# Kernel tuning notes

Hardware: AMD Instinct MI355X
Metric: run time of the kernel (lower is better)

Reference implementation:

```python
import jax, jax.numpy as jnp
import numpy as np

N, D, NUM_CLASSES = 8192, 128, 128
ALPHA = 1.0
K = 16


def setup_inputs() -> dict:
    key = jax.random.key(0)
    k1, k2 = jax.random.split(key)
    inputs = jax.random.normal(k1, (N, D), dtype=jnp.float32)
    targets = jax.random.randint(k2, (N,), 0, NUM_CLASSES, dtype=jnp.int64)
    return {"inputs": inputs, "targets": targets}


def knn_softmax(inputs, targets, alpha=ALPHA, k=K):
    n = inputs.shape[0]
    # pairwise euclidean distances (GEMM-based), clamped like the original
    sq = jnp.sum(inputs * inputs, axis=1)                      # [n]
    d2 = sq[:, None] + sq[None, :] - 2.0 * (inputs @ inputs.T)  # [n,n]
    dist = jnp.sqrt(jnp.maximum(d2, 1e-12))

    eye = jnp.eye(n, dtype=bool)
    same = targets[:, None] == targets[None, :]
    pos_mask = same & ~eye          # same label, off-diagonal
    neg_mask = ~same                # different label (diagonal excluded automatically)

    # per-row threshold: (K+1)-th smallest off-diagonal distance
    dm = jnp.where(eye, jnp.inf, dist)
    neg_topk, _ = jax.lax.top_k(-dm, k + 1)   # k+1 smallest (negated)
    thr = -neg_topk[:, k]                      # [n]

    below = dist < thr[:, None]
    pos_sel = pos_mask & below
    neg_sel = neg_mask & below

    exp_d = jnp.exp(-alpha * dist)
    pos_logit = jnp.sum(jnp.where(pos_sel, exp_d, 0.0), axis=1)  # [n]
    neg_logit = jnp.sum(jnp.where(neg_sel, exp_d, 0.0), axis=1)  # [n]
    count_pos = jnp.sum(pos_sel, axis=1)
    count_neg = jnp.sum(neg_sel, axis=1)

    # fallback when no positive falls below the threshold: use the first positive pair
    first_pos = jnp.argmax(pos_mask, axis=1)                     # [n]
    fb_dist = jnp.take_along_axis(dist, first_pos[:, None], axis=1)[:, 0]
    fallback = jnp.exp(-alpha * fb_dist)
    pos_eff = jnp.where(count_pos == 0, fallback, pos_logit)

    # rows with no positives or no negatives at all are skipped (`continue`)
    valid = pos_mask.any(axis=1) & neg_mask.any(axis=1)

    loss_i = -jnp.log(pos_eff / (pos_eff + neg_logit))
    loss = jnp.sum(jnp.where(valid, loss_i, 0.0)) / n

    count_pos_acc = jnp.where(count_pos == 0, 1, count_pos)  # fallback gives len 1
    accuracy = jnp.sum((valid & (count_pos_acc > count_neg)).astype(jnp.float32)) / n
    tp = jnp.sum(jnp.where(valid, count_pos, 0)).astype(jnp.float32) / n
    tn = jnp.sum(jnp.where(valid, count_neg, 0)).astype(jnp.float32) / n
    return loss, accuracy, tp, tn


def reference(inputs, targets):
    return knn_softmax(inputs, targets)
```

## Files before the change

### kernel.cpp

```cpp
#include <hip/hip_runtime.h>

#define NPTS 8192
#define DIM 128
#define NCLS 128
#define KSEL 17
#define RB   64
#define NIT  32
#define CAPW 40
#define SEG  32
#define NSEG 8
#define MBLK 1024
#define BIG 3.0e38f

typedef short bf16x8 __attribute__((ext_vector_type(8)));
typedef float f32x4 __attribute__((ext_vector_type(4)));

__device__ __forceinline__ unsigned short f2bf(float f) {
  unsigned int u = __float_as_uint(f);
  u += 0x7fffu + ((u >> 16) & 1u);
  return (unsigned short)(u >> 16);
}

__device__ __forceinline__ unsigned flipF(float f) {
  unsigned u = __float_as_uint(f);
  return (u & 0x80000000u) ? ~u : (u | 0x80000000u);
}
__device__ __forceinline__ float unflipF(unsigned k) {
  unsigned u = (k & 0x80000000u) ? (k & 0x7fffffffu) : ~k;
  return __uint_as_float(u);
}

__device__ __forceinline__ float kth17_4(float a, float b, float c, float d) {
  const unsigned ka = flipF(a), kb = flipF(b), kc = flipF(c), kd = flipF(d);
  unsigned ans = 0x80000000u;
  for (int bit = 30; bit >= 0; --bit) {
    unsigned mid = ans | (1u << bit);
    int cc = __popcll(__ballot(ka < mid)) + __popcll(__ballot(kb < mid)) +
             __popcll(__ballot(kc < mid)) + __popcll(__ballot(kd < mid));
    if (cc < KSEL) ans = mid;
  }
  return unflipF(ans);
}

__global__ void prep(const float* __restrict__ X, const long long* __restrict__ targets,
                     unsigned short* __restrict__ Xb, float* __restrict__ sqv,
                     int* __restrict__ tgt, int* __restrict__ ccount,
                     int* __restrict__ j0a, int* __restrict__ j1a) {
  const int tid = threadIdx.x;
  if (blockIdx.x == 2048) {
    __shared__ int cc[NCLS], c0[NCLS], c1[NCLS];
    if (tid < NCLS) { cc[tid] = 0; c0[tid] = 0x7fffffff; c1[tid] = 0x7fffffff; }
    __syncthreads();
    for (int base = tid * 4; base < NPTS; base += 1024) {
      const long long* p = targets + base;
#pragma unroll
      for (int k = 0; k < 4; k++) {
        int c = (int)p[k];
        tgt[base + k] = c;
        atomicAdd(&cc[c], 1);
        atomicMin(&c0[c], base + k);
      }
    }
    __syncthreads();
    for (int base = tid * 4; base < NPTS; base += 1024) {
#pragma unroll
      for (int k = 0; k < 4; k++) {
        int c = tgt[base + k];
        if (base + k != c0[c]) atomicMin(&c1[c], base + k);
      }
    }
    __syncthreads();
    if (tid < NCLS) { ccount[tid] = cc[tid]; j0a[tid] = c0[tid]; j1a[tid] = c1[tid]; }
    return;
  }
  const int w = tid >> 6, lane = tid & 63;
  const int gw = blockIdx.x * 4 + w;
  const float* xr = X + (size_t)gw * DIM;
  float a = xr[lane], b = xr[lane + 64];
  Xb[(size_t)gw * DIM + lane] = f2bf(a);
  Xb[(size_t)gw * DIM + lane + 64] = f2bf(b);
  float s = a * a + b * b;
#pragma unroll
  for (int off = 32; off; off >>= 1) s += __shfl_xor(s, off);
  if (lane == 0) sqv[gw] = s;
}

__global__ __launch_bounds__(256, 4) void knn_main(
    const unsigned short* __restrict__ Xb, const float* __restrict__ sqv,
    const int* __restrict__ tgt, float* __restrict__ scr, int* __restrict__ cscr) {
  __shared__ __align__(16) unsigned short shB[2][4096];
  __shared__ __align__(16) float shPub[RB * CAPW];
  __shared__ int cntL[RB];

  const int tid = threadIdx.x;
  const int w = tid >> 6;
  const int lane = tid & 63;
  const int quad = lane >> 4;
  const int l16 = lane & 15;
  const int rg = blockIdx.x >> 3;
  const int eighth = blockIdx.x & 7;
  const int rbase = rg * RB;
  const int cbase = eighth * 1024;

  const int w0off = (tid << 5) ^ (((tid >> 3) & 7) << 4);
  const unsigned lmlt = (1u << l16) - 1;
  int rdoff[4];
#pragma unroll
  for (int kb = 0; kb < 4; kb++)
    rdoff[kb] = (l16 * 256 + quad * 16 + kb * 64) ^ ((l16 & 7) << 4);

  bf16x8 afrag[4];
  {
    const unsigned short* arow = Xb + (size_t)(rbase + w * 16 + l16) * DIM + quad * 8;
#pragma unroll
    for (int kb = 0; kb < 4; kb++) afrag[kb] = *(const bf16x8*)(arow + kb * 32);
  }
  float sqi[4]; int ti[4];
#pragma unroll
  for (int r = 0; r < 4; r++) {
    int rr = rbase + w * 16 + quad * 4 + r;
    sqi[r] = sqv[rr]; ti[r] = tgt[rr];
  }
  int tdw;
  {
    int d = rbase + w * 16 - cbase;
    tdw = (d >= 0 && d < 1024) ? (d >> 4) : -1;
  }

  const unsigned short* gtile0 = Xb + (size_t)cbase * DIM;
  const float* sqp = sqv + cbase + l16;
  const int*   tgp = tgt + cbase + l16;

  float m1[4], m2[4];
#pragma unroll
  for (int r = 0; r < 4; r++) { m1[r] = BIG; m2[r] = BIG; }
  {
    bf16x8 s0 = *(const bf16x8*)(gtile0 + tid * 16);
    bf16x8 s1 = *(const bf16x8*)(gtile0 + tid * 16 + 8);
    *(bf16x8*)((char*)&shB[0][0] + w0off) = s0;
    *(bf16x8*)((char*)&shB[0][0] + (w0off ^ 16)) = s1;
  }
  float sq0 = sqp[0], sq1 = sqp[16];
  __syncthreads();
  for (int j = 0; j < NIT; j++) {
    const int jn = (j + 1) & (NIT - 1);
    const unsigned short* src = gtile0 + (size_t)jn * 4096;
    bf16x8 s0 = *(const bf16x8*)(src + tid * 16);
    bf16x8 s1 = *(const bf16x8*)(src + tid * 16 + 8);
    const float nsq0 = sqp[jn * 32], nsq1 = sqp[jn * 32 + 16];
    const char* lb = (const char*)&shB[j & 1][0];
    bf16x8 b0[4], b1[4];
#pragma unroll
    for (int kb = 0; kb < 4; kb++) {
      b0[kb] = *(const bf16x8*)(lb + rdoff[kb]);
      b1[kb] = *(const bf16x8*)(lb + rdoff[kb] + 4096);
    }
    f32x4 a0 = {0.f, 0.f, 0.f, 0.f}, a1 = {0.f, 0.f, 0.f, 0.f};
#pragma unroll
    for (int kb = 0; kb < 4; kb++) {
      a0 = __builtin_amdgcn_mfma_f32_16x16x32_bf16(afrag[kb], b0[kb], a0, 0, 0, 0);
      a1 = __builtin_amdgcn_mfma_f32_16x16x32_bf16(afrag[kb], b1[kb], a1, 0, 0, 0);
    }
    float v0[4], v1[4];
#pragma unroll
    for (int r = 0; r < 4; r++) {
      v0[r] = fmaf(-2.0f, a0[r], sq0);
      v1[r] = fmaf(-2.0f, a1[r], sq1);
    }
    if ((unsigned)(tdw - 2 * j) < 2u) {
#pragma unroll
      for (int r = 0; r < 4; r++) {
        if (2 * j == tdw && l16 == quad * 4 + r) v0[r] = BIG;
        if (2 * j + 1 == tdw && l16 == quad * 4 + r) v1[r] = BIG;
      }
    }
#pragma unroll
    for (int r = 0; r < 4; r++) {
      m2[r] = fminf(m2[r], fmaxf(m1[r], v0[r]));
      m1[r] = fminf(m1[r], v0[r]);
      m2[r] = fminf(m2[r], fmaxf(m1[r], v1[r]));
      m1[r] = fminf(m1[r], v1[r]);
    }
    sq0 = nsq0; sq1 = nsq1;
    char* wb = (char*)&shB[(j & 1) ^ 1][0];
    *(bf16x8*)(wb + w0off) = s0;
    *(bf16x8*)(wb + (w0off ^ 16)) = s1;
    __syncthreads();
  }

#pragma unroll
  for (int r = 0; r < 4; r++) {
    const int row = w * 16 + quad * 4 + r;
    shPub[row * 32 + l16 * 2] = m1[r];
    shPub[row * 32 + l16 * 2 + 1] = m2[r];
  }
  __syncthreads();
  float Ur[4] = {0.f, 0.f, 0.f, 0.f};
  for (int rp = 0; rp < 16; rp += 2) {
    const int li = lane & 31;
    const unsigned ka = (lane < 32) ? flipF(shPub[(w * 16 + rp) * 32 + li]) : 0xFFFFFFFFu;
    const unsigned kb2 = (lane < 32) ? flipF(shPub[(w * 16 + rp + 1) * 32 + li]) : 0xFFFFFFFFu;
    unsigned ansA = 0u, ansB = 0u;
    for (int bit = 31; bit >= 14; --bit) {
      const unsigned mA = ansA | (1u << bit), mB = ansB | (1u << bit);
      const int ca = __popcll(__ballot(ka < mA));
      const int cb = __popcll(__ballot(kb2 < mB));
      if (ca < KSEL) ansA = mA;
      if (cb < KSEL) ansB = mB;
    }
    const float ua = unflipF(ansA | 0x3FFFu), ub = unflipF(ansB | 0x3FFFu);
#pragma unroll
    for (int r = 0; r < 4; r++) {
      const int myrow = quad * 4 + r;
      if (myrow == rp) Ur[r] = ua;
      if (myrow == rp + 1) Ur[r] = ub;
    }
  }

  float* bufD = shPub;
  int cntr[4] = {0, 0, 0, 0};
  {
    bf16x8 s0 = *(const bf16x8*)(gtile0 + tid * 16);
    bf16x8 s1 = *(const bf16x8*)(gtile0 + tid * 16 + 8);
    *(bf16x8*)((char*)&shB[0][0] + w0off) = s0;
    *(bf16x8*)((char*)&shB[0][0] + (w0off ^ 16)) = s1;
  }
  sq0 = sqp[0]; sq1 = sqp[16];
  int tj0 = tgp[0], tj1 = tgp[16];
  __syncthreads();
  for (int j = 0; j < NIT; j++) {
    const int jn = (j + 1) & (NIT - 1);
    const unsigned short* src = gtile0 + (size_t)jn * 4096;
    bf16x8 s0 = *(const bf16x8*)(src + tid * 16);
    bf16x8 s1 = *(const bf16x8*)(src + tid * 16 + 8);
    const float nsq0 = sqp[jn * 32], nsq1 = sqp[jn * 32 + 16];
    const int ntj0 = tgp[jn * 32], ntj1 = tgp[jn * 32 + 16];
    const char* lb = (const char*)&shB[j & 1][0];
    bf16x8 b0[4], b1[4];
#pragma unroll
    for (int kb = 0; kb < 4; kb++) {
      b0[kb] = *(const bf16x8*)(lb + rdoff[kb]);
      b1[kb] = *(const bf16x8*)(lb + rdoff[kb] + 4096);
    }
    f32x4 a0 = {0.f, 0.f, 0.f, 0.f}, a1 = {0.f, 0.f, 0.f, 0.f};
#pragma unroll
    for (int kb = 0; kb < 4; kb++) {
      a0 = __builtin_amdgcn_mfma_f32_16x16x32_bf16(afrag[kb], b0[kb], a0, 0, 0, 0);
      a1 = __builtin_amdgcn_mfma_f32_16x16x32_bf16(afrag[kb], b1[kb], a1, 0, 0, 0);
    }
    float v0[4], v1[4];
#pragma unroll
    for (int r = 0; r < 4; r++) {
      v0[r] = fmaf(-2.0f, a0[r], sq0);
      v1[r] = fmaf(-2.0f, a1[r], sq1);
    }
    if ((unsigned)(tdw - 2 * j) < 2u) {
#pragma unroll
      for (int r = 0; r < 4; r++) {
        if (2 * j == tdw && l16 == quad * 4 + r) v0[r] = BIG;
        if (2 * j + 1 == tdw && l16 == quad * 4 + r) v1[r] = BIG;
      }
    }
#pragma unroll
    for (int r = 0; r < 4; r++) {
      {
        const bool p = (v0[r] <= Ur[r]);
        const unsigned long long bal = __ballot(p);
        if (bal) {
          const unsigned qm = (unsigned)(bal >> (quad << 4)) & 0xFFFFu;
          const int pos = cntr[r] + __popc(qm & lmlt);
          if (p && pos < CAPW) {
            unsigned enc = __float_as_uint(fmaxf(v0[r] + sqi[r], 0.0f));
            if (tj0 == ti[r]) enc |= 0x80000000u;
            bufD[(w * 16 + quad * 4 + r) * CAPW + pos] = __uint_as_float(enc);
          }
          cntr[r] += __popc(qm);
        }
      }
      {
        const bool p = (v1[r] <= Ur[r]);
        const unsigned long long bal = __ballot(p);
        if (bal) {
          const unsigned qm = (unsigned)(bal >> (quad << 4)) & 0xFFFFu;
          const int pos = cntr[r] + __popc(qm & lmlt);
          if (p && pos < CAPW) {
            unsigned enc = __float_as_uint(fmaxf(v1[r] + sqi[r], 0.0f));
            if (tj1 == ti[r]) enc |= 0x80000000u;
            bufD[(w * 16 + quad * 4 + r) * CAPW + pos] = __uint_as_float(enc);
          }
          cntr[r] += __popc(qm);
        }
      }
    }
    sq0 = nsq0; sq1 = nsq1; tj0 = ntj0; tj1 = ntj1;
    char* wb = (char*)&shB[(j & 1) ^ 1][0];
    *(bf16x8*)(wb + w0off) = s0;
    *(bf16x8*)(wb + (w0off ^ 16)) = s1;
    __syncthreads();
  }
#pragma unroll
  for (int r = 0; r < 4; r++)
    if (l16 == 0) cntL[w * 16 + quad * 4 + r] = cntr[r];
  __syncthreads();

  for (int rl = 0; rl < 16; rl++) {
    const int grow = rbase + w * 16 + rl;
    const int tot = cntL[w * 16 + rl];
    float* srow = scr + (size_t)grow * (NSEG * SEG) + eighth * SEG;
    if (tot <= SEG) {
      if (lane < tot) srow[lane] = bufD[(w * 16 + rl) * CAPW + lane];
      if (lane == 0) cscr[grow * NSEG + eighth] = tot;
    } else {
      const int n = min(tot, CAPW);
      float e = BIG; int m = 0;
      if (lane < n) {
        unsigned u = __float_as_uint(bufD[(w * 16 + rl) * CAPW + lane]);
        m = (int)(u >> 31); e = __uint_as_float(u & 0x7fffffffu);
      }
      for (int round = 0; round < KSEL; round++) {
        float vv = e; int idx = lane;
#pragma unroll
        for (int off = 32; off; off >>= 1) {
          float ov = __shfl_xor(vv, off);
          int   oi = __shfl_xor(idx, off);
          if (ov < vv || (ov == vv && oi < idx)) { vv = ov; idx = oi; }
        }
        if (idx == lane) {
          unsigned ub = __float_as_uint(e);
          if (m) ub |= 0x80000000u;
          srow[round] = __uint_as_float(ub);
          e = BIG;
        }
      }
      if (lane == 0) cscr[grow * NSEG + eighth] = KSEL;
    }
  }
}

__global__ __launch_bounds__(256) void knn_merge(
    const float* __restrict__ scr, const int* __restrict__ cscr,
    const float* __restrict__ sqv, const int* __restrict__ tgt,
    const int* __restrict__ ccount, const int* __restrict__ j0a,
    const int* __restrict__ j1a, const float* __restrict__ X32,
    float* __restrict__ pacc) {
  __shared__ float blockAcc[4];
  const int tid = threadIdx.x;
  const int w = tid >> 6;
  const int lane = tid & 63;
  if (tid < 4) blockAcc[tid] = 0.0f;
  __syncthreads();
  for (int ri = 0; ri < 2; ri++) {
    const int grow = blockIdx.x * 8 + w * 2 + ri;
    const float* srow = scr + (size_t)grow * (NSEG * SEG);
    const int h = lane >> 5, li = lane & 31;
    float e[4]; int mm[4];
#pragma unroll
    for (int j = 0; j < 4; j++) {
      const int seg = j * 2 + h;
      const int cj = cscr[grow * NSEG + seg];
      if (li < cj) {
        unsigned u = __float_as_uint(srow[seg * SEG + li]);
        mm[j] = (int)(u >> 31); e[j] = __uint_as_float(u & 0x7fffffffu);
      } else { e[j] = BIG; mm[j] = 0; }
    }
    const float t17 = kth17_4(e[0], e[1], e[2], e[3]);
    float pls = 0.0f, nls = 0.0f; int cp = 0, cn = 0;
#pragma unroll
    for (int j = 0; j < 4; j++) {
      const bool s = (e[j] < t17);
      const float x = s ? expf(-sqrtf(fmaxf(e[j], 1e-12f))) : 0.0f;
      if (mm[j]) { pls += x; cp += (int)s; }
      else       { nls += x; cn += (int)s; }
    }
    int cpn = cp * 65536 + cn;
#pragma unroll
    for (int off = 32; off; off >>= 1) {
      pls += __shfl_xor(pls, off); nls += __shfl_xor(nls, off);
      cpn += __shfl_xor(cpn, off);
    }
    const int cpt = cpn >> 16, cnt_ = cpn & 0xffff;
    const int c = tgt[grow];
    const int ncl = ccount[c];
    const bool valid = (ncl > 1) && (ncl < NPTS);
    if (valid) {
      float pos_eff;
      if (cpt == 0) {
        const int jf = (grow == j0a[c]) ? j1a[c] : j0a[c];
        const float* xi = X32 + (size_t)grow * DIM;
        const float* xj = X32 + (size_t)jf * DIM;
        float pp = xi[lane] * xj[lane] + xi[lane + 64] * xj[lane + 64];
#pragma unroll
        for (int off = 32; off; off >>= 1) pp += __shfl_xor(pp, off);
        const float fb2 = sqv[grow] + sqv[jf] - 2.0f * pp;
        pos_eff = expf(-sqrtf(fmaxf(fb2, 1e-12f)));
      } else {
        pos_eff = pls;
      }
      if (lane == 0) {
        const float loss_i = -logf(pos_eff / (pos_eff + nls));
        const int cpa = (cpt == 0) ? 1 : cpt;
        atomicAdd(&blockAcc[0], loss_i);
        atomicAdd(&blockAcc[1], (cpa > cnt_) ? 1.0f : 0.0f);
        atomicAdd(&blockAcc[2], (float)cpt);
        atomicAdd(&blockAcc[3], (float)cnt_);
      }
    }
  }
  __syncthreads();
  if (tid < 4) pacc[blockIdx.x * 4 + tid] = blockAcc[tid];
}

__global__ void fin(const float* __restrict__ pacc, float* __restrict__ out) {
  __shared__ float red[256];
  const int tid = threadIdx.x;
  const int c = tid & 3, b0 = tid >> 2;
  float s = 0.0f;
  for (int b = b0; b < MBLK; b += 64) s += pacc[b * 4 + c];
  red[tid] = s;
  __syncthreads();
  if (tid < 4) {
    float t = 0.0f;
    for (int i = tid; i < 256; i += 4) t += red[i];
    out[tid] = t * (1.0f / (float)NPTS);
  }
}

extern "C" void kernel_launch(void* const* d_in, const int* in_sizes, int n_in,
                              void* d_out, int out_size, void* d_ws, size_t ws_size,
                              hipStream_t stream) {
  const float* X = (const float*)d_in[0];
  const long long* targets = (const long long*)d_in[1];
  float* out = (float*)d_out;

  char* ws = (char*)d_ws;
  unsigned short* Xb = (unsigned short*)ws;
  float* sqv    = (float*)   (ws + (2u << 20));
  int*   tgt    = (int*)     (ws + (2u << 20) + (32u << 10));
  int*   ccount = (int*)     (ws + (2u << 20) + (64u << 10));
  int*   j0a    = (int*)     (ws + (2u << 20) + (65u << 10));
  int*   j1a    = (int*)     (ws + (2u << 20) + (66u << 10));
  float* pacc   = (float*)   (ws + (2u << 20) + (68u << 10));
  float* scr = (float*)(ws + (2u << 20) + (128u << 10));
  int* cscr  = (int*)  (ws + (2u << 20) + (128u << 10) +
                        (size_t)NPTS * NSEG * SEG * 4);

  prep<<<2049, 256, 0, stream>>>(X, targets, Xb, sqv, tgt, ccount, j0a, j1a);
  knn_main<<<1024, 256, 0, stream>>>(Xb, sqv, tgt, scr, cscr);
  knn_merge<<<MBLK, 256, 0, stream>>>(scr, cscr, sqv, tgt, ccount, j0a, j1a, X, pacc);
  fin<<<1, 256, 0, stream>>>(pacc, out);
}
```

Measured before the change: 174.1 us.

## Double row tile per block and stage column tiles via direct global-to-LDS loads

Each block now covers 128 rows instead of 64, so each wave holds two A fragments and reuses every B fragment read from LDS for two MFMAs, halving LDS traffic per MFMA. Column tiles are copied with global_load_lds straight into LDS, with the swizzle moved to the source address, instead of going through registers. The buffer filled in the last iteration of the first pass is reused as the first tile of the second pass. Second-minimum tracking now uses fmed3. In exchange the grid is halved to 512 blocks with launch bounds of 2 blocks per SM, which lowers occupancy and latency hiding and raises register pressure.

```diff
diff --git a/kernel.cpp b/kernel.cpp
--- a/kernel.cpp
+++ b/kernel.cpp
@@ -4,7 +4,7 @@
 #define DIM 128
 #define NCLS 128
 #define KSEL 17
-#define RB   64
+#define RB   128
 #define NIT  32
 #define CAPW 40
 #define SEG  32
@@ -85,7 +85,7 @@
   if (lane == 0) sqv[gw] = s;
 }
 
-__global__ __launch_bounds__(256, 4) void knn_main(
+__global__ __launch_bounds__(256, 2) void knn_main(
     const unsigned short* __restrict__ Xb, const float* __restrict__ sqv,
     const int* __restrict__ tgt, float* __restrict__ scr, int* __restrict__ cscr) {
   __shared__ __align__(16) unsigned short shB[2][4096];
@@ -102,104 +102,132 @@
   const int rbase = rg * RB;
   const int cbase = eighth * 1024;
 
-  const int w0off = (tid << 5) ^ (((tid >> 3) & 7) << 4);
   const unsigned lmlt = (1u << l16) - 1;
   int rdoff[4];
 #pragma unroll
   for (int kb = 0; kb < 4; kb++)
     rdoff[kb] = (l16 * 256 + quad * 16 + kb * 64) ^ ((l16 & 7) << 4);
 
-  bf16x8 afrag[4];
-  {
-    const unsigned short* arow = Xb + (size_t)(rbase + w * 16 + l16) * DIM + quad * 8;
-#pragma unroll
-    for (int kb = 0; kb < 4; kb++) afrag[kb] = *(const bf16x8*)(arow + kb * 32);
-  }
-  float sqi[4]; int ti[4];
-#pragma unroll
-  for (int r = 0; r < 4; r++) {
-    int rr = rbase + w * 16 + quad * 4 + r;
-    sqi[r] = sqv[rr]; ti[r] = tgt[rr];
-  }
-  int tdw;
-  {
-    int d = rbase + w * 16 - cbase;
-    tdw = (d >= 0 && d < 1024) ? (d >> 4) : -1;
-  }
-
-  const unsigned short* gtile0 = Xb + (size_t)cbase * DIM;
+  const int g0 = w * 128 + lane;
+  const int g1 = w * 128 + 64 + lane;
+  const int soff0 = (g0 ^ ((g0 >> 4) & 7)) * 16;
+  const int soff1 = (g1 ^ ((g1 >> 4) & 7)) * 16;
+  const int ldst0 = (w * 128) * 16;
+  const int ldst1 = (w * 128 + 64) * 16;
+
+  const char* gslab0 = (const char*)(Xb) + (size_t)cbase * DIM * 2;
+  auto stage = [&](int buf, int j) {
+    const char* src = gslab0 + (size_t)j * 8192;
+    __builtin_amdgcn_global_load_lds((const unsigned int*)(src + soff0),
+                                     (unsigned int*)((char*)&shB[buf][0] + ldst0),
+                                     16, 0, 0);
+    __builtin_amdgcn_global_load_lds((const unsigned int*)(src + soff1),
+                                     (unsigned int*)((char*)&shB[buf][0] + ldst1),
+                                     16, 0, 0);
+  };
+
+  bf16x8 afrag[2][4];
+#pragma unroll
+  for (int s = 0; s < 2; s++) {
+    const unsigned short* arow =
+        Xb + (size_t)(rbase + w * 32 + s * 16 + l16) * DIM + quad * 8;
+#pragma unroll
+    for (int kb = 0; kb < 4; kb++) afrag[s][kb] = *(const bf16x8*)(arow + kb * 32);
+  }
+  float sqi[2][4]; int ti[2][4];
+#pragma unroll
+  for (int s = 0; s < 2; s++)
+#pragma unroll
+    for (int r = 0; r < 4; r++) {
+      int rr = rbase + w * 32 + s * 16 + quad * 4 + r;
+      sqi[s][r] = sqv[rr]; ti[s][r] = tgt[rr];
+    }
+  int tdw[2];
+#pragma unroll
+  for (int s = 0; s < 2; s++) {
+    int d = rbase + w * 32 + s * 16 - cbase;
+    tdw[s] = (d >= 0 && d < 1024) ? (d >> 4) : -1;
+  }
+
   const float* sqp = sqv + cbase + l16;
   const int*   tgp = tgt + cbase + l16;
 
-  float m1[4], m2[4];
-#pragma unroll
-  for (int r = 0; r < 4; r++) { m1[r] = BIG; m2[r] = BIG; }
-  {
-    bf16x8 s0 = *(const bf16x8*)(gtile0 + tid * 16);
-    bf16x8 s1 = *(const bf16x8*)(gtile0 + tid * 16 + 8);
-    *(bf16x8*)((char*)&shB[0][0] + w0off) = s0;
-    *(bf16x8*)((char*)&shB[0][0] + (w0off ^ 16)) = s1;
-  }
-  float sq0 = sqp[0], sq1 = sqp[16];
+  float m1[2][4], m2[2][4];
+#pragma unroll
+  for (int s = 0; s < 2; s++)
+#pragma unroll
+    for (int r = 0; r < 4; r++) { m1[s][r] = BIG; m2[s][r] = BIG; }
+  stage(0, 0);
   __syncthreads();
   for (int j = 0; j < NIT; j++) {
-    const int jn = (j + 1) & (NIT - 1);
-    const unsigned short* src = gtile0 + (size_t)jn * 4096;
-    bf16x8 s0 = *(const bf16x8*)(src + tid * 16);
-    bf16x8 s1 = *(const bf16x8*)(src + tid * 16 + 8);
-    const float nsq0 = sqp[jn * 32], nsq1 = sqp[jn * 32 + 16];
+    const int jn = (j + 1 < NIT) ? j + 1 : 0;
+    stage((j & 1) ^ 1, jn);
+    const float sq0 = sqp[j * 32], sq1 = sqp[j * 32 + 16];
     const char* lb = (const char*)&shB[j & 1][0];
-    bf16x8 b0[4], b1[4];
-#pragma unroll
-    for (int kb = 0; kb < 4; kb++) {
-      b0[kb] = *(const bf16x8*)(lb + rdoff[kb]);
-      b1[kb] = *(const bf16x8*)(lb + rdoff[kb] + 4096);
-    }
-    f32x4 a0 = {0.f, 0.f, 0.f, 0.f}, a1 = {0.f, 0.f, 0.f, 0.f};
-#pragma unroll
-    for (int kb = 0; kb < 4; kb++) {
-      a0 = __builtin_amdgcn_mfma_f32_16x16x32_bf16(afrag[kb], b0[kb], a0, 0, 0, 0);
-      a1 = __builtin_amdgcn_mfma_f32_16x16x32_bf16(afrag[kb], b1[kb], a1, 0, 0, 0);
-    }
-    float v0[4], v1[4];
+    f32x4 a00 = {0.f,0.f,0.f,0.f}, a10 = {0.f,0.f,0.f,0.f};
+    f32x4 a01 = {0.f,0.f,0.f,0.f}, a11 = {0.f,0.f,0.f,0.f};
+    {
+      bf16x8 b[4];
+#pragma unroll
+      for (int kb = 0; kb < 4; kb++) b[kb] = *(const bf16x8*)(lb + rdoff[kb]);
+#pragma unroll
+      for (int kb = 0; kb < 4; kb++) {
+        a00 = __builtin_amdgcn_mfma_f32_16x16x32_bf16(afrag[0][kb], b[kb], a00, 0, 0, 0);
+        a10 = __builtin_amdgcn_mfma_f32_16x16x32_bf16(afrag[1][kb], b[kb], a10, 0, 0, 0);
+      }
+    }
+    {
+      bf16x8 b[4];
+#pragma unroll
+      for (int kb = 0; kb < 4; kb++) b[kb] = *(const bf16x8*)(lb + rdoff[kb] + 4096);
+#pragma unroll
+      for (int kb = 0; kb < 4; kb++) {
+        a01 = __builtin_amdgcn_mfma_f32_16x16x32_bf16(afrag[0][kb], b[kb], a01, 0, 0, 0);
+        a11 = __builtin_amdgcn_mfma_f32_16x16x32_bf16(afrag[1][kb], b[kb], a11, 0, 0, 0);
+      }
+    }
+    float v0[2][4], v1[2][4];
+#pragma unroll
+    for (int s = 0; s < 2; s++)
+#pragma unroll
+      for (int r = 0; r < 4; r++) {
+        v0[s][r] = fmaf(-2.0f, s ? a10[r] : a00[r], sq0);
+        v1[s][r] = fmaf(-2.0f, s ? a11[r] : a01[r], sq1);
+      }
+    if (((unsigned)(tdw[0] - 2 * j) < 2u) || ((unsigned)(tdw[1] - 2 * j) < 2u)) {
+#pragma unroll
+      for (int s = 0; s < 2; s++)
+#pragma unroll
+        for (int r = 0; r < 4; r++) {
+          if (2 * j == tdw[s] && l16 == quad * 4 + r) v0[s][r] = BIG;
+          if (2 * j + 1 == tdw[s] && l16 == quad * 4 + r) v1[s][r] = BIG;
+        }
+    }
+#pragma unroll
+    for (int s = 0; s < 2; s++)
+#pragma unroll
+      for (int r = 0; r < 4; r++) {
+        m2[s][r] = __builtin_amdgcn_fmed3f(m1[s][r], m2[s][r], v0[s][r]);
+        m1[s][r] = fminf(m1[s][r], v0[s][r]);
+        m2[s][r] = __builtin_amdgcn_fmed3f(m1[s][r], m2[s][r], v1[s][r]);
+        m1[s][r] = fminf(m1[s][r], v1[s][r]);
+      }
+    __syncthreads();
+  }
+
+#pragma unroll
+  for (int s = 0; s < 2; s++)
 #pragma unroll
     for (int r = 0; r < 4; r++) {
-      v0[r] = fmaf(-2.0f, a0[r], sq0);
-      v1[r] = fmaf(-2.0f, a1[r], sq1);
-    }
-    if ((unsigned)(tdw - 2 * j) < 2u) {
-#pragma unroll
-      for (int r = 0; r < 4; r++) {
-        if (2 * j == tdw && l16 == quad * 4 + r) v0[r] = BIG;
-        if (2 * j + 1 == tdw && l16 == quad * 4 + r) v1[r] = BIG;
-      }
-    }
-#pragma unroll
-    for (int r = 0; r < 4; r++) {
-      m2[r] = fminf(m2[r], fmaxf(m1[r], v0[r]));
-      m1[r] = fminf(m1[r], v0[r]);
-      m2[r] = fminf(m2[r], fmaxf(m1[r], v1[r]));
-      m1[r] = fminf(m1[r], v1[r]);
-    }
-    sq0 = nsq0; sq1 = nsq1;
-    char* wb = (char*)&shB[(j & 1) ^ 1][0];
-    *(bf16x8*)(wb + w0off) = s0;
-    *(bf16x8*)(wb + (w0off ^ 16)) = s1;
-    __syncthreads();
-  }
-
-#pragma unroll
-  for (int r = 0; r < 4; r++) {
-    const int row = w * 16 + quad * 4 + r;
-    shPub[row * 32 + l16 * 2] = m1[r];
-    shPub[row * 32 + l16 * 2 + 1] = m2[r];
-  }
-  __syncthreads();
-  float Ur[4] = {0.f, 0.f, 0.f, 0.f};
-  for (int rp = 0; rp < 16; rp += 2) {
+      const int row = w * 32 + s * 16 + quad * 4 + r;
+      shPub[row * 32 + l16 * 2] = m1[s][r];
+      shPub[row * 32 + l16 * 2 + 1] = m2[s][r];
+    }
+  float Ur[2][4];
+  for (int rp = 0; rp < 32; rp += 2) {
     const int li = lane & 31;
-    const unsigned ka = (lane < 32) ? flipF(shPub[(w * 16 + rp) * 32 + li]) : 0xFFFFFFFFu;
-    const unsigned kb2 = (lane < 32) ? flipF(shPub[(w * 16 + rp + 1) * 32 + li]) : 0xFFFFFFFFu;
+    const unsigned ka  = (lane < 32) ? flipF(shPub[(w * 32 + rp) * 32 + li]) : 0xFFFFFFFFu;
+    const unsigned kb2 = (lane < 32) ? flipF(shPub[(w * 32 + rp + 1) * 32 + li]) : 0xFFFFFFFFu;
     unsigned ansA = 0u, ansB = 0u;
     for (int bit = 31; bit >= 14; --bit) {
       const unsigned mA = ansA | (1u << bit), mB = ansB | (1u << bit);
@@ -210,111 +238,121 @@
     }
     const float ua = unflipF(ansA | 0x3FFFu), ub = unflipF(ansB | 0x3FFFu);
 #pragma unroll
-    for (int r = 0; r < 4; r++) {
-      const int myrow = quad * 4 + r;
-      if (myrow == rp) Ur[r] = ua;
-      if (myrow == rp + 1) Ur[r] = ub;
-    }
+    for (int s = 0; s < 2; s++)
+#pragma unroll
+      for (int r = 0; r < 4; r++) {
+        const int myrow = s * 16 + quad * 4 + r;
+        if (myrow == rp) Ur[s][r] = ua;
+        if (myrow == rp + 1) Ur[s][r] = ub;
+      }
   }
 
   float* bufD = shPub;
-  int cntr[4] = {0, 0, 0, 0};
-  {
-    bf16x8 s0 = *(const bf16x8*)(gtile0 + tid * 16);
-    bf16x8 s1 = *(const bf16x8*)(gtile0 + tid * 16 + 8);
-    *(bf16x8*)((char*)&shB[0][0] + w0off) = s0;
-    *(bf16x8*)((char*)&shB[0][0] + (w0off ^ 16)) = s1;
-  }
-  sq0 = sqp[0]; sq1 = sqp[16];
-  int tj0 = tgp[0], tj1 = tgp[16];
+  int cntr[2][4];
+#pragma unroll
+  for (int s = 0; s < 2; s++)
+#pragma unroll
+    for (int r = 0; r < 4; r++) cntr[s][r] = 0;
+  for (int j = 0; j < NIT; j++) {
+    const int jn = (j + 1 < NIT) ? j + 1 : 0;
+    stage((j & 1) ^ 1, jn);
+    const float sq0 = sqp[j * 32], sq1 = sqp[j * 32 + 16];
+    const int tj0 = tgp[j * 32], tj1 = tgp[j * 32 + 16];
+    const char* lb = (const char*)&shB[j & 1][0];
+    f32x4 a00 = {0.f,0.f,0.f,0.f}, a10 = {0.f,0.f,0.f,0.f};
+    f32x4 a01 = {0.f,0.f,0.f,0.f}, a11 = {0.f,0.f,0.f,0.f};
+    {
+      bf16x8 b[4];
+#pragma unroll
+      for (int kb = 0; kb < 4; kb++) b[kb] = *(const bf16x8*)(lb + rdoff[kb]);
+#pragma unroll
+      for (int kb = 0; kb < 4; kb++) {
+        a00 = __builtin_amdgcn_mfma_f32_16x16x32_bf16(afrag[0][kb], b[kb], a00, 0, 0, 0);
+        a10 = __builtin_amdgcn_mfma_f32_16x16x32_bf16(afrag[1][kb], b[kb], a10, 0, 0, 0);
+      }
+    }
+    {
+      bf16x8 b[4];
+#pragma unroll
+      for (int kb = 0; kb < 4; kb++) b[kb] = *(const bf16x8*)(lb + rdoff[kb] + 4096);
+#pragma unroll
+      for (int kb = 0; kb < 4; kb++) {
+        a01 = __builtin_amdgcn_mfma_f32_16x16x32_bf16(afrag[0][kb], b[kb], a01, 0, 0, 0);
+        a11 = __builtin_amdgcn_mfma_f32_16x16x32_bf16(afrag[1][kb], b[kb], a11, 0, 0, 0);
+      }
+    }
+    float v0[2][4], v1[2][4];
+#pragma unroll
+    for (int s = 0; s < 2; s++)
+#pragma unroll
+      for (int r = 0; r < 4; r++) {
+        v0[s][r] = fmaf(-2.0f, s ? a10[r] : a00[r], sq0);
+        v1[s][r] = fmaf(-2.0f, s ? a11[r] : a01[r], sq1);
+      }
+    if (((unsigned)(tdw[0] - 2 * j) < 2u) || ((unsigned)(tdw[1] - 2 * j) < 2u)) {
+#pragma unroll
+      for (int s = 0; s < 2; s++)
+#pragma unroll
+        for (int r = 0; r < 4; r++) {
+          if (2 * j == tdw[s] && l16 == quad * 4 + r) v0[s][r] = BIG;
+          if (2 * j + 1 == tdw[s] && l16 == quad * 4 + r) v1[s][r] = BIG;
+        }
+    }
+#pragma unroll
+    for (int s = 0; s < 2; s++)
+#pragma unroll
+      for (int r = 0; r < 4; r++) {
+        {
+          const bool p = (v0[s][r] <= Ur[s][r]);
+          const unsigned long long bal = __ballot(p);
+          if (bal) {
+            const unsigned qm = (unsigned)(bal >> (quad << 4)) & 0xFFFFu;
+            const int pos = cntr[s][r] + __popc(qm & lmlt);
+            if (p && pos < CAPW) {
+              unsigned enc = __float_as_uint(fmaxf(v0[s][r] + sqi[s][r], 0.0f));
+              if (tj0 == ti[s][r]) enc |= 0x80000000u;
+              bufD[(w * 32 + s * 16 + quad * 4 + r) * CAPW + pos] = __uint_as_float(enc);
+            }
+            cntr[s][r] += __popc(qm);
+          }
+        }
+        {
+          const bool p = (v1[s][r] <= Ur[s][r]);
+          const unsigned long long bal = __ballot(p);
+          if (bal) {
+            const unsigned qm = (unsigned)(bal >> (quad << 4)) & 0xFFFFu;
+            const int pos = cntr[s][r] + __popc(qm & lmlt);
+            if (p && pos < CAPW) {
+              unsigned enc = __float_as_uint(fmaxf(v1[s][r] + sqi[s][r], 0.0f));
+              if (tj1 == ti[s][r]) enc |= 0x80000000u;
+              bufD[(w * 32 + s * 16 + quad * 4 + r) * CAPW + pos] = __uint_as_float(enc);
+            }
+            cntr[s][r] += __popc(qm);
+          }
+        }
+      }
+    __syncthreads();
+  }
+#pragma unroll
+  for (int s = 0; s < 2; s++)
+#pragma unroll
+    for (int r = 0; r < 4; r++)
+      if (l16 == 0) cntL[w * 32 + s * 16 + quad * 4 + r] = cntr[s][r];
   __syncthreads();
-  for (int j = 0; j < NIT; j++) {
-    const int jn = (j + 1) & (NIT - 1);
-    const unsigned short* src = gtile0 + (size_t)jn * 4096;
-    bf16x8 s0 = *(const bf16x8*)(src + tid * 16);
-    bf16x8 s1 = *(const bf16x8*)(src + tid * 16 + 8);
-    const float nsq0 = sqp[jn * 32], nsq1 = sqp[jn * 32 + 16];
-    const int ntj0 = tgp[jn * 32], ntj1 = tgp[jn * 32 + 16];
-    const char* lb = (const char*)&shB[j & 1][0];
-    bf16x8 b0[4], b1[4];
-#pragma unroll
-    for (int kb = 0; kb < 4; kb++) {
-      b0[kb] = *(const bf16x8*)(lb + rdoff[kb]);
-      b1[kb] = *(const bf16x8*)(lb + rdoff[kb] + 4096);
-    }
-    f32x4 a0 = {0.f, 0.f, 0.f, 0.f}, a1 = {0.f, 0.f, 0.f, 0.f};
-#pragma unroll
-    for (int kb = 0; kb < 4; kb++) {
-      a0 = __builtin_amdgcn_mfma_f32_16x16x32_bf16(afrag[kb], b0[kb], a0, 0, 0, 0);
-      a1 = __builtin_amdgcn_mfma_f32_16x16x32_bf16(afrag[kb], b1[kb], a1, 0, 0, 0);
-    }
-    float v0[4], v1[4];
-#pragma unroll
-    for (int r = 0; r < 4; r++) {
-      v0[r] = fmaf(-2.0f, a0[r], sq0);
-      v1[r] = fmaf(-2.0f, a1[r], sq1);
-    }
-    if ((unsigned)(tdw - 2 * j) < 2u) {
-#pragma unroll
-      for (int r = 0; r < 4; r++) {
-        if (2 * j == tdw && l16 == quad * 4 + r) v0[r] = BIG;
-        if (2 * j + 1 == tdw && l16 == quad * 4 + r) v1[r] = BIG;
-      }
-    }
-#pragma unroll
-    for (int r = 0; r < 4; r++) {
-      {
-        const bool p = (v0[r] <= Ur[r]);
-        const unsigned long long bal = __ballot(p);
-        if (bal) {
-          const unsigned qm = (unsigned)(bal >> (quad << 4)) & 0xFFFFu;
-          const int pos = cntr[r] + __popc(qm & lmlt);
-          if (p && pos < CAPW) {
-            unsigned enc = __float_as_uint(fmaxf(v0[r] + sqi[r], 0.0f));
-            if (tj0 == ti[r]) enc |= 0x80000000u;
-            bufD[(w * 16 + quad * 4 + r) * CAPW + pos] = __uint_as_float(enc);
-          }
-          cntr[r] += __popc(qm);
-        }
-      }
-      {
-        const bool p = (v1[r] <= Ur[r]);
-        const unsigned long long bal = __ballot(p);
-        if (bal) {
-          const unsigned qm = (unsigned)(bal >> (quad << 4)) & 0xFFFFu;
-          const int pos = cntr[r] + __popc(qm & lmlt);
-          if (p && pos < CAPW) {
-            unsigned enc = __float_as_uint(fmaxf(v1[r] + sqi[r], 0.0f));
-            if (tj1 == ti[r]) enc |= 0x80000000u;
-            bufD[(w * 16 + quad * 4 + r) * CAPW + pos] = __uint_as_float(enc);
-          }
-          cntr[r] += __popc(qm);
-        }
-      }
-    }
-    sq0 = nsq0; sq1 = nsq1; tj0 = ntj0; tj1 = ntj1;
-    char* wb = (char*)&shB[(j & 1) ^ 1][0];
-    *(bf16x8*)(wb + w0off) = s0;
-    *(bf16x8*)(wb + (w0off ^ 16)) = s1;
-    __syncthreads();
-  }
-#pragma unroll
-  for (int r = 0; r < 4; r++)
-    if (l16 == 0) cntL[w * 16 + quad * 4 + r] = cntr[r];
-  __syncthreads();
-
-  for (int rl = 0; rl < 16; rl++) {
-    const int grow = rbase + w * 16 + rl;
-    const int tot = cntL[w * 16 + rl];
+
+  for (int rl = 0; rl < 32; rl++) {
+    const int row = w * 32 + rl;
+    const int grow = rbase + row;
+    const int tot = cntL[row];
     float* srow = scr + (size_t)grow * (NSEG * SEG) + eighth * SEG;
     if (tot <= SEG) {
-      if (lane < tot) srow[lane] = bufD[(w * 16 + rl) * CAPW + lane];
+      if (lane < tot) srow[lane] = bufD[row * CAPW + lane];
       if (lane == 0) cscr[grow * NSEG + eighth] = tot;
     } else {
       const int n = min(tot, CAPW);
       float e = BIG; int m = 0;
       if (lane < n) {
-        unsigned u = __float_as_uint(bufD[(w * 16 + rl) * CAPW + lane]);
+        unsigned u = __float_as_uint(bufD[row * CAPW + lane]);
         m = (int)(u >> 31); e = __uint_as_float(u & 0x7fffffffu);
       }
       for (int round = 0; round < KSEL; round++) {
@@ -445,7 +483,7 @@
                         (size_t)NPTS * NSEG * SEG * 4);
 
   prep<<<2049, 256, 0, stream>>>(X, targets, Xb, sqv, tgt, ccount, j0a, j1a);
-  knn_main<<<1024, 256, 0, stream>>>(Xb, sqv, tgt, scr, cscr);
+  knn_main<<<512, 256, 0, stream>>>(Xb, sqv, tgt, scr, cscr);
   knn_merge<<<MBLK, 256, 0, stream>>>(scr, cscr, sqv, tgt, ccount, j0a, j1a, X, pacc);
   fin<<<1, 256, 0, stream>>>(pacc, out);
 }
```

Result: slower. 189.9 us (+9.1%).

## Stage B tiles via direct global-to-LDS loads and use med3 for top-2 update

Applied to the files above, without the earlier changes.

Replaces the register-staged global→LDS copy of the column tiles with __builtin_amdgcn_global_load_lds direct loads, issued one tile ahead into the double buffer. The XOR swizzle moves from the LDS write address to the global source address. The sq and target values are now loaded for the current tile rather than prefetched. It also replaces the min/max pair in the running top-2 update with fmed3, splits the B fragment reads into two halves to lower register pressure, and drops one barrier between the min pass and the threshold search. This is meant to cut VGPR use and per-iteration copy instructions, but it relies on the async LDS loads being visible after the barrier and on the barrier removal being safe.

```diff
diff --git a/kernel.cpp b/kernel.cpp
--- a/kernel.cpp
+++ b/kernel.cpp
@@ -102,12 +102,29 @@
   const int rbase = rg * RB;
   const int cbase = eighth * 1024;
 
-  const int w0off = (tid << 5) ^ (((tid >> 3) & 7) << 4);
   const unsigned lmlt = (1u << l16) - 1;
   int rdoff[4];
 #pragma unroll
   for (int kb = 0; kb < 4; kb++)
     rdoff[kb] = (l16 * 256 + quad * 16 + kb * 64) ^ ((l16 & 7) << 4);
+
+  const int g0 = w * 128 + lane;
+  const int g1 = w * 128 + 64 + lane;
+  const int soff0 = (g0 ^ ((g0 >> 4) & 7)) * 16;
+  const int soff1 = (g1 ^ ((g1 >> 4) & 7)) * 16;
+  const int ldst0 = (w * 128) * 16;
+  const int ldst1 = (w * 128 + 64) * 16;
+
+  const char* gslab0 = (const char*)(Xb) + (size_t)cbase * DIM * 2;
+  auto stage = [&](int buf, int j) {
+    const char* src = gslab0 + (size_t)j * 8192;
+    __builtin_amdgcn_global_load_lds((const unsigned int*)(src + soff0),
+                                     (unsigned int*)((char*)&shB[buf][0] + ldst0),
+                                     16, 0, 0);
+    __builtin_amdgcn_global_load_lds((const unsigned int*)(src + soff1),
+                                     (unsigned int*)((char*)&shB[buf][0] + ldst1),
+                                     16, 0, 0);
+  };
 
   bf16x8 afrag[4];
   {
@@ -127,39 +144,35 @@
     tdw = (d >= 0 && d < 1024) ? (d >> 4) : -1;
   }
 
-  const unsigned short* gtile0 = Xb + (size_t)cbase * DIM;
   const float* sqp = sqv + cbase + l16;
   const int*   tgp = tgt + cbase + l16;
 
   float m1[4], m2[4];
 #pragma unroll
   for (int r = 0; r < 4; r++) { m1[r] = BIG; m2[r] = BIG; }
-  {
-    bf16x8 s0 = *(const bf16x8*)(gtile0 + tid * 16);
-    bf16x8 s1 = *(const bf16x8*)(gtile0 + tid * 16 + 8);
-    *(bf16x8*)((char*)&shB[0][0] + w0off) = s0;
-    *(bf16x8*)((char*)&shB[0][0] + (w0off ^ 16)) = s1;
-  }
-  float sq0 = sqp[0], sq1 = sqp[16];
+  stage(0, 0);
   __syncthreads();
   for (int j = 0; j < NIT; j++) {
-    const int jn = (j + 1) & (NIT - 1);
-    const unsigned short* src = gtile0 + (size_t)jn * 4096;
-    bf16x8 s0 = *(const bf16x8*)(src + tid * 16);
-    bf16x8 s1 = *(const bf16x8*)(src + tid * 16 + 8);
-    const float nsq0 = sqp[jn * 32], nsq1 = sqp[jn * 32 + 16];
+    const int jn = (j + 1 < NIT) ? j + 1 : 0;
+    stage((j & 1) ^ 1, jn);
+    const float sq0 = sqp[j * 32], sq1 = sqp[j * 32 + 16];
     const char* lb = (const char*)&shB[j & 1][0];
-    bf16x8 b0[4], b1[4];
-#pragma unroll
-    for (int kb = 0; kb < 4; kb++) {
-      b0[kb] = *(const bf16x8*)(lb + rdoff[kb]);
-      b1[kb] = *(const bf16x8*)(lb + rdoff[kb] + 4096);
-    }
     f32x4 a0 = {0.f, 0.f, 0.f, 0.f}, a1 = {0.f, 0.f, 0.f, 0.f};
-#pragma unroll
-    for (int kb = 0; kb < 4; kb++) {
-      a0 = __builtin_amdgcn_mfma_f32_16x16x32_bf16(afrag[kb], b0[kb], a0, 0, 0, 0);
-      a1 = __builtin_amdgcn_mfma_f32_16x16x32_bf16(afrag[kb], b1[kb], a1, 0, 0, 0);
+    {
+      bf16x8 b[4];
+#pragma unroll
+      for (int kb = 0; kb < 4; kb++) b[kb] = *(const bf16x8*)(lb + rdoff[kb]);
+#pragma unroll
+      for (int kb = 0; kb < 4; kb++)
+        a0 = __builtin_amdgcn_mfma_f32_16x16x32_bf16(afrag[kb], b[kb], a0, 0, 0, 0);
+    }
+    {
+      bf16x8 b[4];
+#pragma unroll
+      for (int kb = 0; kb < 4; kb++) b[kb] = *(const bf16x8*)(lb + rdoff[kb] + 4096);
+#pragma unroll
+      for (int kb = 0; kb < 4; kb++)
+        a1 = __builtin_amdgcn_mfma_f32_16x16x32_bf16(afrag[kb], b[kb], a1, 0, 0, 0);
     }
     float v0[4], v1[4];
 #pragma unroll
@@ -176,15 +189,11 @@
     }
 #pragma unroll
     for (int r = 0; r < 4; r++) {
-      m2[r] = fminf(m2[r], fmaxf(m1[r], v0[r]));
+      m2[r] = __builtin_amdgcn_fmed3f(m1[r], m2[r], v0[r]);
       m1[r] = fminf(m1[r], v0[r]);
-      m2[r] = fminf(m2[r], fmaxf(m1[r], v1[r]));
+      m2[r] = __builtin_amdgcn_fmed3f(m1[r], m2[r], v1[r]);
       m1[r] = fminf(m1[r], v1[r]);
     }
-    sq0 = nsq0; sq1 = nsq1;
-    char* wb = (char*)&shB[(j & 1) ^ 1][0];
-    *(bf16x8*)(wb + w0off) = s0;
-    *(bf16x8*)(wb + (w0off ^ 16)) = s1;
     __syncthreads();
   }
 
@@ -194,11 +203,10 @@
     shPub[row * 32 + l16 * 2] = m1[r];
     shPub[row * 32 + l16 * 2 + 1] = m2[r];
   }
-  __syncthreads();
-  float Ur[4] = {0.f, 0.f, 0.f, 0.f};
+  float Ur[4];
   for (int rp = 0; rp < 16; rp += 2) {
     const int li = lane & 31;
-    const unsigned ka = (lane < 32) ? flipF(shPub[(w * 16 + rp) * 32 + li]) : 0xFFFFFFFFu;
+    const unsigned ka  = (lane < 32) ? flipF(shPub[(w * 16 + rp) * 32 + li]) : 0xFFFFFFFFu;
     const unsigned kb2 = (lane < 32) ? flipF(shPub[(w * 16 + rp + 1) * 32 + li]) : 0xFFFFFFFFu;
     unsigned ansA = 0u, ansB = 0u;
     for (int bit = 31; bit >= 14; --bit) {
@@ -216,37 +224,32 @@
       if (myrow == rp + 1) Ur[r] = ub;
     }
   }
+  __syncthreads();
 
   float* bufD = shPub;
   int cntr[4] = {0, 0, 0, 0};
-  {
-    bf16x8 s0 = *(const bf16x8*)(gtile0 + tid * 16);
-    bf16x8 s1 = *(const bf16x8*)(gtile0 + tid * 16 + 8);
-    *(bf16x8*)((char*)&shB[0][0] + w0off) = s0;
-    *(bf16x8*)((char*)&shB[0][0] + (w0off ^ 16)) = s1;
-  }
-  sq0 = sqp[0]; sq1 = sqp[16];
-  int tj0 = tgp[0], tj1 = tgp[16];
-  __syncthreads();
   for (int j = 0; j < NIT; j++) {
-    const int jn = (j + 1) & (NIT - 1);
-    const unsigned short* src = gtile0 + (size_t)jn * 4096;
-    bf16x8 s0 = *(const bf16x8*)(src + tid * 16);
-    bf16x8 s1 = *(const bf16x8*)(src + tid * 16 + 8);
-    const float nsq0 = sqp[jn * 32], nsq1 = sqp[jn * 32 + 16];
-    const int ntj0 = tgp[jn * 32], ntj1 = tgp[jn * 32 + 16];
+    const int jn = (j + 1 < NIT) ? j + 1 : 0;
+    stage((j & 1) ^ 1, jn);
+    const float sq0 = sqp[j * 32], sq1 = sqp[j * 32 + 16];
+    const int tj0 = tgp[j * 32], tj1 = tgp[j * 32 + 16];
     const char* lb = (const char*)&shB[j & 1][0];
-    bf16x8 b0[4], b1[4];
-#pragma unroll
-    for (int kb = 0; kb < 4; kb++) {
-      b0[kb] = *(const bf16x8*)(lb + rdoff[kb]);
-      b1[kb] = *(const bf16x8*)(lb + rdoff[kb] + 4096);
-    }
     f32x4 a0 = {0.f, 0.f, 0.f, 0.f}, a1 = {0.f, 0.f, 0.f, 0.f};
-#pragma unroll
-    for (int kb = 0; kb < 4; kb++) {
-      a0 = __builtin_amdgcn_mfma_f32_16x16x32_bf16(afrag[kb], b0[kb], a0, 0, 0, 0);
-      a1 = __builtin_amdgcn_mfma_f32_16x16x32_bf16(afrag[kb], b1[kb], a1, 0, 0, 0);
+    {
+      bf16x8 b[4];
+#pragma unroll
+      for (int kb = 0; kb < 4; kb++) b[kb] = *(const bf16x8*)(lb + rdoff[kb]);
+#pragma unroll
+      for (int kb = 0; kb < 4; kb++)
+        a0 = __builtin_amdgcn_mfma_f32_16x16x32_bf16(afrag[kb], b[kb], a0, 0, 0, 0);
+    }
+    {
+      bf16x8 b[4];
+#pragma unroll
+      for (int kb = 0; kb < 4; kb++) b[kb] = *(const bf16x8*)(lb + rdoff[kb] + 4096);
+#pragma unroll
+      for (int kb = 0; kb < 4; kb++)
+        a1 = __builtin_amdgcn_mfma_f32_16x16x32_bf16(afrag[kb], b[kb], a1, 0, 0, 0);
     }
     float v0[4], v1[4];
 #pragma unroll
@@ -292,10 +295,6 @@
         }
       }
     }
-    sq0 = nsq0; sq1 = nsq1; tj0 = ntj0; tj1 = ntj1;
-    char* wb = (char*)&shB[(j & 1) ^ 1][0];
-    *(bf16x8*)(wb + w0off) = s0;
-    *(bf16x8*)(wb + (w0off ^ 16)) = s1;
     __syncthreads();
   }
 #pragma unroll
@@ -304,17 +303,18 @@
   __syncthreads();
 
   for (int rl = 0; rl < 16; rl++) {
-    const int grow = rbase + w * 16 + rl;
-    const int tot = cntL[w * 16 + rl];
+    const int row = w * 16 + rl;
+    const int grow = rbase + row;
+    const int tot = cntL[row];
     float* srow = scr + (size_t)grow * (NSEG * SEG) + eighth * SEG;
     if (tot <= SEG) {
-      if (lane < tot) srow[lane] = bufD[(w * 16 + rl) * CAPW + lane];
+      if (lane < tot) srow[lane] = bufD[row * CAPW + lane];
       if (lane == 0) cscr[grow * NSEG + eighth] = tot;
     } else {
       const int n = min(tot, CAPW);
       float e = BIG; int m = 0;
       if (lane < n) {
-        unsigned u = __float_as_uint(bufD[(w * 16 + rl) * CAPW + lane]);
+        unsigned u = __float_as_uint(bufD[row * CAPW + lane]);
         m = (int)(u >> 31); e = __uint_as_float(u & 0x7fffffffu);
       }
       for (int round = 0; round < KSEL; round++) {
```

Result: no change. 174.3 us (+0.1%).
